# Optimization experiments

Measured on AMD Instinct MI355X. Metric: run time of the kernel, lower is better.

## Reference

```python
import jax, jax.numpy as jnp
import numpy as np
from jax import lax

B, C, H, W = 32, 32, 64, 64
K = 1024
DN_T = ('NCHW', 'IOHW', 'NCHW')  # conv_transpose: kernel [in, out, kh, kw]
DN_C = ('NCHW', 'OIHW', 'NCHW')  # conv:           kernel [out, in, kh, kw]


def setup_inputs() -> dict:
    key = jax.random.key(0)
    ks = jax.random.split(key, 8)
    return {
        'z': jax.random.normal(ks[0], (B, C, H, W), jnp.float32),
        'codebook': jax.random.normal(ks[1], (K, C), jnp.float32),
        'w1': jax.random.normal(ks[2], (32, 128, 4, 4), jnp.float32) * 0.05,
        'b1': jnp.zeros((128,), jnp.float32),
        'w2': jax.random.normal(ks[3], (128, 64, 4, 4), jnp.float32) * 0.05,
        'b2': jnp.zeros((64,), jnp.float32),
        'w3': jax.random.normal(ks[4], (3, 64, 3, 3), jnp.float32) * 0.05,
        'b3': jnp.zeros((3,), jnp.float32),
    }


def _quantize(z, codebook):
    # z: [B, C, H, W] -> flat [N, C]
    zf = jnp.transpose(z, (0, 2, 3, 1)).reshape(-1, z.shape[1])
    # squared distances: ||z||^2 - 2 z.E^T + ||E||^2  -> [N, K]
    d = (jnp.sum(zf * zf, axis=1, keepdims=True)
         - 2.0 * zf @ codebook.T
         + jnp.sum(codebook * codebook, axis=1))
    idx = jnp.argmin(d, axis=1)                      # [N]
    q = codebook[idx].reshape(z.shape[0], z.shape[2], z.shape[3], z.shape[1])
    q = jnp.transpose(q, (0, 3, 1, 2))               # [B, C, H, W]
    # straight-through estimator
    return z + lax.stop_gradient(q - z)


def _decode(q, w1, b1, w2, b2, w3, b3):
    x = lax.conv_transpose(q, w1, strides=(2, 2), padding='SAME',
                           dimension_numbers=DN_T) + b1[None, :, None, None]
    x = jax.nn.relu(x)                               # [B, 128, 2H, 2W]
    x = lax.conv_transpose(x, w2, strides=(2, 2), padding='SAME',
                           dimension_numbers=DN_T) + b2[None, :, None, None]
    x = jax.nn.relu(x)                               # [B, 64, 4H, 4W]
    x = lax.conv_general_dilated(x, w3, window_strides=(1, 1), padding='SAME',
                                 dimension_numbers=DN_C) + b3[None, :, None, None]
    return jax.nn.sigmoid(x)                         # [B, 3, 4H, 4W]


def reference(z, codebook, w1, b1, w2, b2, w3, b3):
    q = _quantize(z, codebook)
    return _decode(q, w1, b1, w2, b2, w3, b3)
```

## Files before the change

kernel.cpp:

```cpp
#include <hip/hip_runtime.h>
#include <hip/hip_bf16.h>


typedef __attribute__((ext_vector_type(8)))  short  bf16x8;
typedef __attribute__((ext_vector_type(4)))  float  f32x4;
typedef __attribute__((ext_vector_type(16))) float  f32x16;

static constexpr int B_=32, C_=32, H_=64, W_=64, K_=1024;
static constexpr int NPOS = B_*H_*W_;

__device__ __forceinline__ unsigned short f2bf(float f){
  unsigned u = __float_as_uint(f);
  u = u + 0x7FFFu + ((u>>16)&1u);
  return (unsigned short)(u>>16);
}
__device__ __forceinline__ float bf2f(unsigned short h){
  return __uint_as_float(((unsigned)h)<<16);
}
__device__ __forceinline__ f32x16 mfma32(bf16x8 a, bf16x8 b, f32x16 c){
  return __builtin_amdgcn_mfma_f32_32x32x16_bf16(a,b,c,0,0,0);
}
__device__ __forceinline__ f32x4 mfma16(bf16x8 a, bf16x8 b, f32x4 c){
  return __builtin_amdgcn_mfma_f32_16x16x32_bf16(a,b,c,0,0,0);
}
__device__ __forceinline__ void gload16(const void* g, void* l){
  __builtin_amdgcn_global_load_lds(
      (const __attribute__((address_space(1))) void*)(unsigned long long)g,
      (__attribute__((address_space(3))) void*)(unsigned)(unsigned long long)l,
      16, 0, 0);
}

__global__ __launch_bounds__(256) void prep_kernel(
    const float* __restrict__ cb, const float* __restrict__ w1,
    const float* __restrict__ w2, const float* __restrict__ w3,
    double* __restrict__ cb64, double* __restrict__ e2,
    unsigned short* __restrict__ cbp_hi, unsigned short* __restrict__ cbp_lo,
    float* __restrict__ e2h,
    unsigned short* __restrict__ wt1p, unsigned short* __restrict__ wt2p,
    unsigned short* __restrict__ w3p, float* __restrict__ zpage,
    int* __restrict__ cnt) {
  int idx = blockIdx.x*256 + threadIdx.x;
  if (idx == 0) cnt[0] = 0;
  if (idx < 64) zpage[idx] = 0.f;
  if (idx < K_*C_) {
    float v = cb[idx];
    cb64[idx] = (double)v;
    unsigned short h = f2bf(v);
    cbp_hi[idx] = h;
    cbp_lo[idx] = f2bf(v - bf2f(h));
  }
  if (idx < K_) {
    double s = 0.0;
    #pragma unroll
    for (int c=0;c<C_;++c){ double v=(double)cb[idx*C_+c]; s+=v*v; }
    e2[idx] = s;
    e2h[idx] = -0.5f * (float)s;
  }
  if (idx < 65536) {
    int e=idx&7, lane=(idx>>3)&63, g=(idx>>9)&3, t=(idx>>11)&3, c=(idx>>13)&1, p=idx>>14;
    int ic = c*16 + (lane>>5)*8 + e;
    int oc = g*32 + (lane&31);
    int ky = 2*(t>>1) + (p>>1), kx = 2*(t&1) + (p&1);
    wt1p[idx] = f2bf(w1[((ic*128+oc)*4+ky)*4+kx]);
  }
  if (idx < 131072) {
    int e=idx&7, lane=(idx>>3)&63, g=(idx>>9)&1, t=(idx>>10)&3, c=(idx>>12)&3, m=(idx>>14)&1, p=idx>>15;
    int ic = m*64 + c*16 + (lane>>5)*8 + e;
    int oc = g*32 + (lane&31);
    int ky = 2*(t>>1) + (p>>1), kx = 2*(t&1) + (p&1);
    wt2p[idx] = f2bf(w2[((ic*64+oc)*4+ky)*4+kx]);
  }
  if (idx < 9216) {
    int e=idx&7, lane=(idx>>3)&63, c=(idx>>9)&1, t=idx>>10;
    int ic = c*32 + ((lane>>4)&3)*8 + e;
    int oc = lane&15;
    int dy = t/3, dx = t - 3*dy;
    w3p[idx] = (oc<3) ? f2bf(w3[((oc*64+ic)*3+dy)*3+dx]) : (unsigned short)0;
  }
}

__global__ __launch_bounds__(256) void zprep_kernel(
    const float* __restrict__ z, unsigned short* __restrict__ zth,
    unsigned short* __restrict__ ztl) {
  int n = blockIdx.x*256 + threadIdx.x;
  int b = n >> 12, hw = n & 4095;
  const float* zp = z + (((size_t)b*C_) << 12) + hw;
  unsigned short th[C_], tl[C_];
  #pragma unroll
  for (int c=0;c<C_;++c) {
    float v = zp[(size_t)c<<12];
    unsigned short h = f2bf(v);
    th[c] = h;
    tl[c] = f2bf(v - bf2f(h));
  }
  bf16x8* dh = (bf16x8*)(zth + (size_t)n*C_);
  bf16x8* dl = (bf16x8*)(ztl + (size_t)n*C_);
  #pragma unroll
  for (int v=0;v<4;++v){ dh[v]=((bf16x8*)th)[v]; dl[v]=((bf16x8*)tl)[v]; }
}

__global__ __launch_bounds__(256) void quantm_kernel(
    const unsigned short* __restrict__ zth, const unsigned short* __restrict__ ztl,
    const unsigned short* __restrict__ cbp_hi, const unsigned short* __restrict__ cbp_lo,
    const float* __restrict__ e2h, const float* __restrict__ cb,
    unsigned short* __restrict__ q, int* __restrict__ cnt, int* __restrict__ list) {
  __shared__ bf16x8 ch[1024], cl[1024];
  __shared__ float  el[256];
  int tid = threadIdx.x, lane = tid&63, wv = tid>>6;
  int m0 = blockIdx.x*128 + wv*32;
  int colL = lane&15, g = lane>>4;

  bf16x8 ah[2], al[2];
  #pragma unroll
  for (int mt=0;mt<2;++mt) {
    int pos = m0 + mt*16 + colL;
    ah[mt] = *(const bf16x8*)(zth + (size_t)pos*C_ + g*8);
    al[mt] = *(const bf16x8*)(ztl + (size_t)pos*C_ + g*8);
  }

  float b1[2][4], b2[2][4]; int i1[2][4];
  #pragma unroll
  for (int mt=0;mt<2;++mt)
    #pragma unroll
    for (int r=0;r<4;++r){ b1[mt][r]=-3e38f; b2[mt][r]=-3e38f; i1[mt][r]=0; }

  for (int cb0 = 0; cb0 < K_; cb0 += 256) {
    __syncthreads();
    {
      const bf16x8* sh = (const bf16x8*)cbp_hi + cb0*4;
      const bf16x8* sl = (const bf16x8*)cbp_lo + cb0*4;
      #pragma unroll
      for (int v=0;v<4;++v){ ch[tid + v*256] = sh[tid + v*256];
                             cl[tid + v*256] = sl[tid + v*256]; }
      el[tid] = e2h[cb0 + tid];
    }
    __syncthreads();
    #pragma unroll
    for (int nt=0; nt<16; ++nt) {
      int cloc = nt*16 + colL;
      float ei = el[cloc];
      bf16x8 bh = ch[cloc*4 + g];
      bf16x8 bl = cl[cloc*4 + g];
      int nidx = cb0 + cloc;
      #pragma unroll
      for (int mt=0;mt<2;++mt) {
        f32x4 acc = {ei, ei, ei, ei};
        acc = mfma16(al[mt], bh, acc);
        acc = mfma16(ah[mt], bl, acc);
        acc = mfma16(ah[mt], bh, acc);
        #pragma unroll
        for (int r=0;r<4;++r) {
          float s = acc[r];
          b2[mt][r] = fmaxf(b2[mt][r], fminf(s, b1[mt][r]));
          if (s > b1[mt][r]) { b1[mt][r] = s; i1[mt][r] = nidx; }
        }
      }
    }
  }

  #pragma unroll
  for (int mask=1; mask<16; mask<<=1) {
    #pragma unroll
    for (int mt=0;mt<2;++mt)
      #pragma unroll
      for (int r=0;r<4;++r) {
        float o1 = __shfl_xor(b1[mt][r], mask);
        float o2 = __shfl_xor(b2[mt][r], mask);
        int   oi = __shfl_xor(i1[mt][r], mask);
        float nb2 = fmaxf(fminf(b1[mt][r], o1), fmaxf(b2[mt][r], o2));
        if (o1 > b1[mt][r]) { b1[mt][r] = o1; i1[mt][r] = oi; }
        b2[mt][r] = nb2;
      }
  }

  #pragma unroll
  for (int mt=0;mt<2;++mt)
    #pragma unroll
    for (int r=0;r<4;++r) {
      int m = m0 + mt*16 + g*4 + r;
      int idx = i1[mt][r];
      unsigned h0 = f2bf(cb[idx*C_ + 2*colL]);
      unsigned h1 = f2bf(cb[idx*C_ + 2*colL + 1]);
      ((unsigned*)q)[(((size_t)(colL>>2))*NPOS + m)*4 + (colL&3)] = h0 | (h1<<16);
      if (colL == 0 && (b1[mt][r] - b2[mt][r]) < 0.02f) {
        int slot = atomicAdd(cnt, 1);
        list[slot] = m;
      }
    }
}

__global__ __launch_bounds__(256) void refine_kernel(
    const int* __restrict__ cnt, const int* __restrict__ list,
    const float* __restrict__ z, const double* __restrict__ cb64,
    const double* __restrict__ e2, const float* __restrict__ cb,
    unsigned short* __restrict__ q) {
  int lane = threadIdx.x & 63;
  int wv = (blockIdx.x*256 + threadIdx.x) >> 6;
  int n_ref = cnt[0];
  for (int w = wv; w < n_ref; w += 1024) {
    int m = list[w];
    int b = m >> 12, hw = m & 4095;
    const float* zp = z + (((size_t)b*C_) << 12) + hw;
    double zr[C_];
    #pragma unroll
    for (int c=0;c<C_;++c) zr[c] = (double)zp[(size_t)c<<12];
    double best = -1e300; int bi = 0;
    for (int kk=0; kk<16; ++kk) {
      int k = kk*64 + lane;
      const double* e = cb64 + k*C_;
      double a0=0,a1=0,a2=0,a3=0;
      #pragma unroll
      for (int c=0;c<C_;c+=4) {
        a0 += zr[c  ]*e[c  ]; a1 += zr[c+1]*e[c+1];
        a2 += zr[c+2]*e[c+2]; a3 += zr[c+3]*e[c+3];
      }
      double s = 2.0*((a0+a1)+(a2+a3)) - e2[k];
      if (s > best) { best = s; bi = k; }
    }
    #pragma unroll
    for (int mask=1; mask<64; mask<<=1) {
      double ob = __shfl_xor(best, mask);
      int    oi = __shfl_xor(bi, mask);
      if (ob > best || (ob == best && oi < bi)) { best = ob; bi = oi; }
    }
    if (lane < 16) {
      unsigned h0 = f2bf(cb[bi*C_ + 2*lane]);
      unsigned h1 = f2bf(cb[bi*C_ + 2*lane + 1]);
      ((unsigned*)q)[(((size_t)(lane>>2))*NPOS + m)*4 + (lane&3)] = h0 | (h1<<16);
    }
  }
}

__global__ __launch_bounds__(256) void convt1_kernel(
    const unsigned short* __restrict__ q, const unsigned short* __restrict__ wt1p,
    const float* __restrict__ b1, const float* __restrict__ zpage,
    unsigned short* __restrict__ x1, int b0) {
  __shared__ unsigned short At[4*4*34*8];
  int tid = threadIdx.x;
  int p = tid>>6, py=(tid>>7)&1, px=(tid>>6)&1;
  int lane = tid&63, xi = lane&31, half = lane>>5, ocl = lane&31;
  int bl = blockIdx.z, b = b0 + bl;
  int Y0 = blockIdx.y*2, X0 = blockIdx.x*32;

  for (int s = tid; s < 544; s += 256) {
    int t = (s*1928)>>16;
    int c = s - t*34;
    int r = t & 3, k8 = t >> 2;
    int hg = Y0-1+r, wg = X0-1+c;
    const unsigned short* src =
        (hg>=0 && hg<64 && wg>=0 && wg<64)
            ? q + ((size_t)k8*NPOS + ((b<<12) + hg*64 + wg))*8
            : (const unsigned short*)zpage;
    *(bf16x8*)&At[s*8] = *(const bf16x8*)src;
  }
  __syncthreads();

  f32x16 acc[2][4];
  #pragma unroll
  for (int g=0;g<4;++g){
    float bv = b1[g*32+ocl];
    #pragma unroll
    for (int yr=0;yr<2;++yr){
      #pragma unroll
      for (int r=0;r<16;++r) acc[yr][g][r]=bv;
    }
  }

  #pragma unroll
  for (int c16=0;c16<2;++c16) {
    #pragma unroll
    for (int t=0;t<4;++t) {
      int j=t>>1, kx=t&1;
      int col = xi+px+kx;
      int rb = (c16*2+half)*4 + py + j;
      bf16x8 a0 = *(const bf16x8*)&At[((rb+0)*34+col)*8];
      bf16x8 a1 = *(const bf16x8*)&At[((rb+1)*34+col)*8];
      const unsigned short* wb = wt1p + ((size_t)(((p*2+c16)*4+t)*4)*64 + lane)*8;
      #pragma unroll
      for (int g=0;g<4;++g) {
        bf16x8 bf = *(const bf16x8*)(wb + g*512);
        acc[0][g] = mfma32(a0, bf, acc[0][g]);
        acc[1][g] = mfma32(a1, bf, acc[1][g]);
      }
    }
  }

  #pragma unroll
  for (int yr=0;yr<2;++yr) {
    int Y = 2*(Y0+yr)+py;
    #pragma unroll
    for (int g=0;g<4;++g) {
      int oc = g*32 + ocl, cg = oc>>3, o8 = oc&7;
      unsigned short* dst = x1 + ((((size_t)bl*16 + cg)*128 + Y)*128 + (2*X0+px))*8 + o8;
      #pragma unroll
      for (int r=0;r<16;++r) {
        int xo = (r&3) + 8*(r>>2) + 4*half;
        dst[(size_t)xo*16] = f2bf(fmaxf(acc[yr][g][r], 0.f));
      }
    }
  }
}

__global__ __launch_bounds__(512, 4) void convt2_kernel(
    const unsigned short* __restrict__ x1, const unsigned short* __restrict__ wt2p,
    const float* __restrict__ b2, const float* __restrict__ zpage,
    unsigned short* __restrict__ x2) {
  __shared__ unsigned short At[2][1664*8];
  int tid = threadIdx.x;
  int wv = __builtin_amdgcn_readfirstlane(tid>>6);
  int lane = tid&63;
  int p = wv>>1, yh = wv&1;
  int py = p>>1, px = p&1;
  int xi = lane&31, half = lane>>5, ocl = lane&31;
  int bl = blockIdx.z;
  int Y0 = blockIdx.y*4, X0 = blockIdx.x*32;

  auto stage = [&](int m, int buf) {
    const unsigned short* xsrc = x1 + ((size_t)bl*16 + m*8)*128*128*8;
    #pragma unroll
    for (int it = 0; it < 4; ++it) {
      int sbase = it*512 + wv*64;
      if (sbase < 1664) {
        int s = sbase + lane;
        int t = (s*1928)>>16;
        int c = s - t*34;
        int k8 = (t*43)>>8;
        int r = t - k8*6;
        int hg = Y0-1+r, wg = X0-1+c;
        bool v = (s < 1632) && hg>=0 && hg<128 && wg>=0 && wg<128;
        const void* src = v ? (const void*)(xsrc + (((size_t)k8*128 + hg)*128 + wg)*8)
                            : (const void*)zpage;
        gload16(src, (void*)&At[buf][sbase*8]);
      }
    }
  };

  f32x16 acc[2][2];
  #pragma unroll
  for (int g=0;g<2;++g){
    float bv = b2[g*32+ocl];
    #pragma unroll
    for (int yr=0;yr<2;++yr){
      #pragma unroll
      for (int r=0;r<16;++r) acc[yr][g][r]=bv;
    }
  }

  stage(0, 0);
  __syncthreads();
  stage(1, 1);

  #pragma unroll
  for (int m=0;m<2;++m) {
    if (m == 1) __syncthreads();
    const unsigned short* Ab = At[m];
    #pragma unroll
    for (int c16=0;c16<4;++c16) {
      #pragma unroll
      for (int t=0;t<4;++t) {
        int j=t>>1, kx=t&1;
        int col = xi+px+kx;
        int rb = (c16*2+half)*6 + py + j + yh*2;
        bf16x8 a0 = *(const bf16x8*)&Ab[((rb+0)*34+col)*8];
        bf16x8 a1 = *(const bf16x8*)&Ab[((rb+1)*34+col)*8];
        const unsigned short* wb = wt2p + ((size_t)(((((p*2+m)*4+c16)*4+t)*2))*64 + lane)*8;
        bf16x8 bf0 = *(const bf16x8*)wb;
        bf16x8 bf1 = *(const bf16x8*)(wb + 512);
        acc[0][0]=mfma32(a0,bf0,acc[0][0]); acc[1][0]=mfma32(a1,bf0,acc[1][0]);
        acc[0][1]=mfma32(a0,bf1,acc[0][1]); acc[1][1]=mfma32(a1,bf1,acc[1][1]);
      }
    }
  }

  #pragma unroll
  for (int yr=0;yr<2;++yr) {
    int Y = 2*(Y0 + yh*2 + yr) + py;
    #pragma unroll
    for (int g=0;g<2;++g) {
      int oc = g*32 + ocl, cg = oc>>3, o8 = oc&7;
      unsigned short* dst = x2 + ((((size_t)bl*8 + cg)*256 + Y)*256 + (2*X0+px))*8 + o8;
      #pragma unroll
      for (int r=0;r<16;++r) {
        int xo = (r&3) + 8*(r>>2) + 4*half;
        dst[(size_t)xo*16] = f2bf(fmaxf(acc[yr][g][r], 0.f));
      }
    }
  }
}

__global__ __launch_bounds__(256) void conv3_kernel(
    const unsigned short* __restrict__ x2, const unsigned short* __restrict__ w3p,
    const float* __restrict__ b3, const float* __restrict__ zpage,
    float* __restrict__ out, int b0) {
  __shared__ unsigned short Xt[4*6*66*8];
  int tid = threadIdx.x, w = tid>>6, lane = tid&63;
  int xi = lane&15, k8A = (lane>>4)&3, oc = lane&15;
  int bl = blockIdx.z, b = b0 + bl;
  int y0 = blockIdx.y*4, x0 = blockIdx.x*64;
  int y = y0 + w;

  f32x4 acc[4];
  float bv = (oc<3) ? b3[oc] : 0.f;
  #pragma unroll
  for (int mt=0;mt<4;++mt){ acc[mt][0]=bv; acc[mt][1]=bv; acc[mt][2]=bv; acc[mt][3]=bv; }

  for (int c=0;c<2;++c) {
    __syncthreads();
    for (int s = tid; s < 1584; s += 256) {
      int t = (s*993)>>16;
      int cc = s - t*66;
      int k8 = (t*43)>>8;
      int r = t - k8*6;
      int rf = y0-1+r, cf = x0-1+cc;
      const unsigned short* src =
          (rf>=0 && rf<256 && cf>=0 && cf<256)
              ? x2 + ((((size_t)bl*8 + c*4 + k8)*256 + rf)*256 + cf)*8
              : (const unsigned short*)zpage;
      *(bf16x8*)&Xt[s*8] = *(const bf16x8*)src;
    }
    __syncthreads();

    #pragma unroll
    for (int t=0;t<9;++t) {
      int dy = t/3, dx = t - 3*dy;
      bf16x8 bf = *(const bf16x8*)(w3p + ((size_t)(t*2+c)*64 + lane)*8);
      #pragma unroll
      for (int mt=0;mt<4;++mt) {
        bf16x8 a = *(const bf16x8*)&Xt[((size_t)(k8A*6 + (w+dy))*66 + (mt*16 + xi + dx))*8];
        acc[mt] = mfma16(a, bf, acc[mt]);
      }
    }
  }

  if (oc < 3) {
    #pragma unroll
    for (int mt=0;mt<4;++mt) {
      f32x4 v;
      #pragma unroll
      for (int r=0;r<4;++r) v[r] = 1.f/(1.f + __expf(-acc[mt][r]));
      int x = x0 + mt*16 + ((lane>>4)&3)*4;
      *(f32x4*)(out + (((size_t)b*3 + oc)*256 + y)*256 + x) = v;
    }
  }
}

extern "C" void kernel_launch(void* const* d_in, const int* in_sizes, int n_in,
                              void* d_out, int out_size, void* d_ws, size_t ws_size,
                              hipStream_t stream) {
  const float* z  = (const float*)d_in[0];
  const float* cb = (const float*)d_in[1];
  const float* w1 = (const float*)d_in[2];
  const float* b1 = (const float*)d_in[3];
  const float* w2 = (const float*)d_in[4];
  const float* b2 = (const float*)d_in[5];
  const float* w3 = (const float*)d_in[6];
  const float* b3 = (const float*)d_in[7];
  float* out = (float*)d_out;

  char* ws = (char*)d_ws;
  size_t off = 0;
  auto alloc = [&](size_t bytes) -> void* {
    void* p = (void*)(ws + off);
    off += (bytes + 255) & ~(size_t)255;
    return p;
  };
  double* cb64         = (double*)alloc((size_t)K_*C_*8);
  double* e2           = (double*)alloc((size_t)K_*8);
  float*  zpage        = (float*)alloc(256);
  unsigned short* cbph = (unsigned short*)alloc((size_t)K_*C_*2);
  unsigned short* cbpl = (unsigned short*)alloc((size_t)K_*C_*2);
  float*  e2h          = (float*)alloc((size_t)K_*4);
  int*    cnt          = (int*)alloc(256);
  int*    list         = (int*)alloc((size_t)NPOS*4);
  unsigned short* zth  = (unsigned short*)alloc((size_t)NPOS*C_*2);
  unsigned short* ztl  = (unsigned short*)alloc((size_t)NPOS*C_*2);
  unsigned short* wt1p = (unsigned short*)alloc((size_t)65536*2);
  unsigned short* wt2p = (unsigned short*)alloc((size_t)131072*2);
  unsigned short* w3p  = (unsigned short*)alloc((size_t)9216*2);
  unsigned short* q    = (unsigned short*)alloc((size_t)NPOS*C_*2);
  size_t fixed = off;

  size_t per_b = ((size_t)16*128*128*8 + (size_t)8*256*256*8) * 2;
  long long avail = (long long)ws_size - (long long)fixed;
  int chunk = (avail >= (long long)per_b) ? (int)(avail / (long long)per_b) : 1;
  if (chunk > B_) chunk = B_;
  unsigned short* x1 = (unsigned short*)alloc((size_t)chunk*16*128*128*8*2);
  unsigned short* x2 = (unsigned short*)alloc((size_t)chunk*8*256*256*8*2);

  prep_kernel<<<512, 256, 0, stream>>>(cb, w1, w2, w3, cb64, e2, cbph, cbpl,
                                       e2h, wt1p, wt2p, w3p, zpage, cnt);
  zprep_kernel<<<512, 256, 0, stream>>>(z, zth, ztl);
  quantm_kernel<<<1024, 256, 0, stream>>>(zth, ztl, cbph, cbpl, e2h, cb,
                                          q, cnt, list);
  refine_kernel<<<256, 256, 0, stream>>>(cnt, list, z, cb64, e2, cb, q);

  for (int b0 = 0; b0 < B_; b0 += chunk) {
    int nb = (B_ - b0 < chunk) ? (B_ - b0) : chunk;
    convt1_kernel<<<dim3(2,32,nb), 256, 0, stream>>>(q, wt1p, b1, zpage, x1, b0);
    convt2_kernel<<<dim3(4,32,nb), 512, 0, stream>>>(x1, wt2p, b2, zpage, x2);
    conv3_kernel <<<dim3(4,64,nb), 256, 0, stream>>>(x2, w3p, b3, zpage, out, b0);
  }
}
```

Baseline: 523.8 us.

## Restructure convt2 work split, stage outputs via LDS, add XCD swizzle

convt2 now gives each wave one 32-channel output group across four rows instead of two groups across two rows, and prefetches its weight fragments into registers ahead of compute. Outputs go to LDS and are then written to global memory as coalesced 16-byte stores, replacing scattered 2-byte stores. Both convt2 and conv3 remap block IDs with an XCD-aware swizzle, and conv3 switches its halo load to direct global-to-LDS loads with a launch-bounds occupancy hint. The register prefetch of sixteen weight vectors raises register pressure, and the LDS staging adds extra barriers.

```diff
diff --git a/kernel.cpp b/kernel.cpp
--- a/kernel.cpp
+++ b/kernel.cpp
@@ -28,6 +28,11 @@
       (const __attribute__((address_space(1))) void*)(unsigned long long)g,
       (__attribute__((address_space(3))) void*)(unsigned)(unsigned long long)l,
       16, 0, 0);
+}
+__device__ __forceinline__ int xcd_swz(int lid, int nwg){
+  int q = nwg >> 3, r = nwg & 7;
+  int xcd = lid & 7, pos = lid >> 3;
+  return (xcd < r ? xcd*(q+1) : r*(q+1) + (xcd-r)*q) + pos;
 }
 
 __global__ __launch_bounds__(256) void prep_kernel(
@@ -305,17 +310,27 @@
     const unsigned short* __restrict__ x1, const unsigned short* __restrict__ wt2p,
     const float* __restrict__ b2, const float* __restrict__ zpage,
     unsigned short* __restrict__ x2) {
-  __shared__ unsigned short At[2][1664*8];
+  __shared__ unsigned short lds[32768];
+  unsigned short* At0 = lds;
+  unsigned short* At1 = lds + 1664*8;
+  unsigned short* Lt  = lds;
+
   int tid = threadIdx.x;
   int wv = __builtin_amdgcn_readfirstlane(tid>>6);
   int lane = tid&63;
-  int p = wv>>1, yh = wv&1;
+  int p = wv>>1, g = wv&1;
   int py = p>>1, px = p&1;
   int xi = lane&31, half = lane>>5, ocl = lane&31;
-  int bl = blockIdx.z;
-  int Y0 = blockIdx.y*4, X0 = blockIdx.x*32;
-
-  auto stage = [&](int m, int buf) {
+
+  int gx = gridDim.x, gy = gridDim.y;
+  int nwg = gx*gy*(int)gridDim.z;
+  int lid = blockIdx.x + gx*(blockIdx.y + gy*blockIdx.z);
+  int swz = xcd_swz(lid, nwg);
+  int bx = swz % gx; int t2 = swz / gx; int by = t2 % gy; int bl = t2 / gy;
+
+  int Y0 = by*4, X0 = bx*32;
+
+  auto stage = [&](int m, unsigned short* buf) {
     const unsigned short* xsrc = x1 + ((size_t)bl*16 + m*8)*128*128*8;
     #pragma unroll
     for (int it = 0; it < 4; ++it) {
@@ -330,73 +345,92 @@
         bool v = (s < 1632) && hg>=0 && hg<128 && wg>=0 && wg<128;
         const void* src = v ? (const void*)(xsrc + (((size_t)k8*128 + hg)*128 + wg)*8)
                             : (const void*)zpage;
-        gload16(src, (void*)&At[buf][sbase*8]);
+        gload16(src, (void*)&buf[sbase*8]);
       }
     }
   };
 
-  f32x16 acc[2][2];
-  #pragma unroll
-  for (int g=0;g<2;++g){
+  f32x16 acc[4];
+  {
     float bv = b2[g*32+ocl];
     #pragma unroll
-    for (int yr=0;yr<2;++yr){
-      #pragma unroll
-      for (int r=0;r<16;++r) acc[yr][g][r]=bv;
-    }
-  }
-
-  stage(0, 0);
-  __syncthreads();
-  stage(1, 1);
-
-  #pragma unroll
-  for (int m=0;m<2;++m) {
-    if (m == 1) __syncthreads();
-    const unsigned short* Ab = At[m];
+    for (int yr=0;yr<4;++yr)
+      #pragma unroll
+      for (int r=0;r<16;++r) acc[yr][r]=bv;
+  }
+
+  bf16x8 wreg[16];
+  auto prefw = [&](int m) {
+    #pragma unroll
+    for (int i=0;i<16;++i) {
+      wreg[i] = *(const bf16x8*)(wt2p +
+          ((size_t)(((((p*2+m)*4+(i>>2))*4+(i&3))*2 + g))*64 + lane)*8);
+    }
+  };
+  auto compute = [&](const unsigned short* Ab) {
     #pragma unroll
     for (int c16=0;c16<4;++c16) {
       #pragma unroll
       for (int t=0;t<4;++t) {
         int j=t>>1, kx=t&1;
         int col = xi+px+kx;
-        int rb = (c16*2+half)*6 + py + j + yh*2;
-        bf16x8 a0 = *(const bf16x8*)&Ab[((rb+0)*34+col)*8];
-        bf16x8 a1 = *(const bf16x8*)&Ab[((rb+1)*34+col)*8];
-        const unsigned short* wb = wt2p + ((size_t)(((((p*2+m)*4+c16)*4+t)*2))*64 + lane)*8;
-        bf16x8 bf0 = *(const bf16x8*)wb;
-        bf16x8 bf1 = *(const bf16x8*)(wb + 512);
-        acc[0][0]=mfma32(a0,bf0,acc[0][0]); acc[1][0]=mfma32(a1,bf0,acc[1][0]);
-        acc[0][1]=mfma32(a0,bf1,acc[0][1]); acc[1][1]=mfma32(a1,bf1,acc[1][1]);
-      }
-    }
-  }
-
-  #pragma unroll
-  for (int yr=0;yr<2;++yr) {
-    int Y = 2*(Y0 + yh*2 + yr) + py;
-    #pragma unroll
-    for (int g=0;g<2;++g) {
-      int oc = g*32 + ocl, cg = oc>>3, o8 = oc&7;
-      unsigned short* dst = x2 + ((((size_t)bl*8 + cg)*256 + Y)*256 + (2*X0+px))*8 + o8;
-      #pragma unroll
-      for (int r=0;r<16;++r) {
-        int xo = (r&3) + 8*(r>>2) + 4*half;
-        dst[(size_t)xo*16] = f2bf(fmaxf(acc[yr][g][r], 0.f));
-      }
-    }
-  }
-}
-
-__global__ __launch_bounds__(256) void conv3_kernel(
+        int rb = (c16*2+half)*6 + py + j;
+        bf16x8 w = wreg[c16*4+t];
+        acc[0] = mfma32(*(const bf16x8*)&Ab[((rb+0)*34+col)*8], w, acc[0]);
+        acc[1] = mfma32(*(const bf16x8*)&Ab[((rb+1)*34+col)*8], w, acc[1]);
+        acc[2] = mfma32(*(const bf16x8*)&Ab[((rb+2)*34+col)*8], w, acc[2]);
+        acc[3] = mfma32(*(const bf16x8*)&Ab[((rb+3)*34+col)*8], w, acc[3]);
+      }
+    }
+  };
+
+  stage(0, At0);
+  prefw(0);
+  __syncthreads();
+  stage(1, At1);
+  compute(At0);
+  prefw(1);
+  __syncthreads();
+  compute(At1);
+
+  __syncthreads();
+  #pragma unroll
+  for (int yr=0;yr<4;++yr) {
+    int ly = 2*yr+py;
+    #pragma unroll
+    for (int r=0;r<16;++r) {
+      int xo = (r&3) + 8*(r>>2) + 4*half;
+      int lx = 2*xo+px;
+      Lt[(ly*64+lx)*64 + g*32 + ocl] = f2bf(fmaxf(acc[yr][r], 0.f));
+    }
+  }
+  __syncthreads();
+  #pragma unroll
+  for (int i=0;i<8;++i) {
+    int u = i*512 + tid;
+    int och8 = u&7, lx = (u>>3)&63, ly = u>>9;
+    unsigned short* dp = x2 +
+        (((size_t)(bl*8+och8)*256 + (2*Y0+ly))*256 + (2*X0+lx))*8;
+    *(bf16x8*)dp = *(const bf16x8*)&Lt[u*8];
+  }
+}
+
+__global__ __launch_bounds__(256, 6) void conv3_kernel(
     const unsigned short* __restrict__ x2, const unsigned short* __restrict__ w3p,
     const float* __restrict__ b3, const float* __restrict__ zpage,
     float* __restrict__ out, int b0) {
-  __shared__ unsigned short Xt[4*6*66*8];
+  __shared__ unsigned short Xt[1600*8];
   int tid = threadIdx.x, w = tid>>6, lane = tid&63;
   int xi = lane&15, k8A = (lane>>4)&3, oc = lane&15;
-  int bl = blockIdx.z, b = b0 + bl;
-  int y0 = blockIdx.y*4, x0 = blockIdx.x*64;
+
+  int gx = gridDim.x, gy = gridDim.y;
+  int nwg = gx*gy*(int)gridDim.z;
+  int lid = blockIdx.x + gx*(blockIdx.y + gy*blockIdx.z);
+  int swz = xcd_swz(lid, nwg);
+  int bx = swz % gx; int t2 = swz / gx; int by = t2 % gy; int bl = t2 / gy;
+
+  int b = b0 + bl;
+  int y0 = by*4, x0 = bx*64;
   int y = y0 + w;
 
   f32x4 acc[4];
@@ -406,17 +440,22 @@
 
   for (int c=0;c<2;++c) {
     __syncthreads();
-    for (int s = tid; s < 1584; s += 256) {
-      int t = (s*993)>>16;
-      int cc = s - t*66;
-      int k8 = (t*43)>>8;
-      int r = t - k8*6;
-      int rf = y0-1+r, cf = x0-1+cc;
-      const unsigned short* src =
-          (rf>=0 && rf<256 && cf>=0 && cf<256)
-              ? x2 + ((((size_t)bl*8 + c*4 + k8)*256 + rf)*256 + cf)*8
-              : (const unsigned short*)zpage;
-      *(bf16x8*)&Xt[s*8] = *(const bf16x8*)src;
+    #pragma unroll
+    for (int it=0; it<7; ++it) {
+      int sbase = it*256 + w*64;
+      if (sbase < 1600) {
+        int s = sbase + lane;
+        int t = (s*993)>>16;
+        int cc = s - t*66;
+        int k8 = (t*43)>>8;
+        int r = t - k8*6;
+        int rf = y0-1+r, cf = x0-1+cc;
+        bool vOK = (s < 1584) && rf>=0 && rf<256 && cf>=0 && cf<256;
+        const void* src = vOK
+            ? (const void*)(x2 + ((((size_t)bl*8 + c*4 + k8)*256 + rf)*256 + cf)*8)
+            : (const void*)zpage;
+        gload16(src, (void*)&Xt[sbase*8]);
+      }
     }
     __syncthreads();
 
```

After: 578.3 us. 1.1x slower.

## Split convt2 LDS staging into four phases with vmcnt-based pipelined waits

Applied to the files above, without the earlier changes.

The convt2 kernel's input staging is split from two half-channel buffers into four quarter-channel phases, issued ahead with async global-to-LDS loads. Full __syncthreads barriers are replaced by explicit s_waitcnt vmcnt counts plus raw s_barrier, so compute on early phases can start while later loads are still in flight. This aims to hide global load latency better at the cost of hand-tuned waitcnt values that depend on the compiler's instruction emission order. The weight loads from global inside compute are also vector memory ops, which could interfere with the vmcnt accounting.

```diff
diff --git a/kernel.cpp b/kernel.cpp
--- a/kernel.cpp
+++ b/kernel.cpp
@@ -28,6 +28,12 @@
       (const __attribute__((address_space(1))) void*)(unsigned long long)g,
       (__attribute__((address_space(3))) void*)(unsigned)(unsigned long long)l,
       16, 0, 0);
+}
+#define WAITVM(N) asm volatile("s_waitcnt vmcnt(" #N ")" ::: "memory")
+__device__ __forceinline__ void barrier_raw(){
+  asm volatile("" ::: "memory");
+  __builtin_amdgcn_s_barrier();
+  asm volatile("" ::: "memory");
 }
 
 __global__ __launch_bounds__(256) void prep_kernel(
@@ -305,7 +311,7 @@
     const unsigned short* __restrict__ x1, const unsigned short* __restrict__ wt2p,
     const float* __restrict__ b2, const float* __restrict__ zpage,
     unsigned short* __restrict__ x2) {
-  __shared__ unsigned short At[2][1664*8];
+  __shared__ unsigned short At[4*1024*8];
   int tid = threadIdx.x;
   int wv = __builtin_amdgcn_readfirstlane(tid>>6);
   int lane = tid&63;
@@ -315,23 +321,22 @@
   int bl = blockIdx.z;
   int Y0 = blockIdx.y*4, X0 = blockIdx.x*32;
 
-  auto stage = [&](int m, int buf) {
-    const unsigned short* xsrc = x1 + ((size_t)bl*16 + m*8)*128*128*8;
-    #pragma unroll
-    for (int it = 0; it < 4; ++it) {
-      int sbase = it*512 + wv*64;
-      if (sbase < 1664) {
-        int s = sbase + lane;
-        int t = (s*1928)>>16;
-        int c = s - t*34;
-        int k8 = (t*43)>>8;
-        int r = t - k8*6;
-        int hg = Y0-1+r, wg = X0-1+c;
-        bool v = (s < 1632) && hg>=0 && hg<128 && wg>=0 && wg<128;
-        const void* src = v ? (const void*)(xsrc + (((size_t)k8*128 + hg)*128 + wg)*8)
-                            : (const void*)zpage;
-        gload16(src, (void*)&At[buf][sbase*8]);
-      }
+  auto issue = [&](int P) {
+    int m = P>>1, h = P&1;
+    const unsigned short* xsrc = x1 + ((size_t)bl*16 + m*8 + h*4)*128*128*8;
+    #pragma unroll
+    for (int it = 0; it < 2; ++it) {
+      int u0 = it*512 + wv*64;
+      int u = u0 + lane;
+      int tl = (u*1928)>>16;
+      int c  = u - tl*34;
+      int k8 = (tl*43)>>8;
+      int r  = tl - k8*6;
+      int hg = Y0-1+r, wg = X0-1+c;
+      bool v = (u < 816) && hg>=0 && hg<128 && wg>=0 && wg<128;
+      const void* src = v ? (const void*)(xsrc + (((size_t)k8*128 + hg)*128 + wg)*8)
+                          : (const void*)zpage;
+      gload16(src, (void*)&At[((size_t)P*1024 + u0)*8]);
     }
   };
 
@@ -340,29 +345,24 @@
   for (int g=0;g<2;++g){
     float bv = b2[g*32+ocl];
     #pragma unroll
-    for (int yr=0;yr<2;++yr){
+    for (int yr=0;yr<2;++yr)
       #pragma unroll
       for (int r=0;r<16;++r) acc[yr][g][r]=bv;
-    }
-  }
-
-  stage(0, 0);
-  __syncthreads();
-  stage(1, 1);
-
-  #pragma unroll
-  for (int m=0;m<2;++m) {
-    if (m == 1) __syncthreads();
-    const unsigned short* Ab = At[m];
-    #pragma unroll
-    for (int c16=0;c16<4;++c16) {
+  }
+
+  auto compute = [&](int P) {
+    int m = P>>1;
+    const unsigned short* Ab = &At[(size_t)P*1024*8];
+    #pragma unroll
+    for (int ci=0; ci<2; ++ci) {
+      int c16 = (P&1)*2 + ci;
       #pragma unroll
       for (int t=0;t<4;++t) {
         int j=t>>1, kx=t&1;
         int col = xi+px+kx;
-        int rb = (c16*2+half)*6 + py + j + yh*2;
-        bf16x8 a0 = *(const bf16x8*)&Ab[((rb+0)*34+col)*8];
-        bf16x8 a1 = *(const bf16x8*)&Ab[((rb+1)*34+col)*8];
+        int lrow = ((c16*2+half)&3)*6 + py + j + yh*2;
+        bf16x8 a0 = *(const bf16x8*)&Ab[((lrow+0)*34+col)*8];
+        bf16x8 a1 = *(const bf16x8*)&Ab[((lrow+1)*34+col)*8];
         const unsigned short* wb = wt2p + ((size_t)(((((p*2+m)*4+c16)*4+t)*2))*64 + lane)*8;
         bf16x8 bf0 = *(const bf16x8*)wb;
         bf16x8 bf1 = *(const bf16x8*)(wb + 512);
@@ -370,7 +370,18 @@
         acc[0][1]=mfma32(a0,bf1,acc[0][1]); acc[1][1]=mfma32(a1,bf1,acc[1][1]);
       }
     }
-  }
+  };
+
+  issue(0); issue(1); issue(2);
+  WAITVM(4); barrier_raw();
+  compute(0);
+  issue(3);
+  WAITVM(4); barrier_raw();
+  compute(1);
+  WAITVM(2); barrier_raw();
+  compute(2);
+  WAITVM(0); barrier_raw();
+  compute(3);
 
   #pragma unroll
   for (int yr=0;yr<2;++yr) {
```

New measurement: 519.1 us. About the same (-0.9%).
